# Performance work log

Hardware: AMD Instinct MI355X
Metric: run time of the kernel (lower is better)

## Reference

```python
import jax, jax.numpy as jnp
import numpy as np
import math

N_NODES = 50000
N_EDGES = 500000
HIDDEN = 64
N_LAYERS = 4
DELTA = 2.5
N_AGG = 6      # mean, max, min, std, var, sum
N_SCALE = 3    # identity, amplification, attenuation
EPS_BN = 1e-5


def setup_inputs() -> dict:
    key = jax.random.key(0)
    ks = jax.random.split(key, 12)
    d = HIDDEN
    L = N_LAYERS
    din_u = (N_AGG * N_SCALE + 1) * d  # 19*d: [self || scaled aggregates]
    return {
        "node_feat": jax.random.normal(ks[0], (N_NODES, d), jnp.float32),
        "edge_feat": jax.random.normal(ks[1], (N_EDGES, 4), jnp.float32),
        "edge_src": jax.random.randint(ks[2], (N_EDGES,), 0, N_NODES, jnp.int32),
        "edge_dst": jax.random.randint(ks[3], (N_EDGES,), 0, N_NODES, jnp.int32),
        "WM": jax.random.normal(ks[4], (L, 2 * d, d), jnp.float32) / math.sqrt(2 * d),
        "bM": jnp.zeros((L, d), jnp.float32),
        "WU": jax.random.normal(ks[5], (L, din_u, d), jnp.float32) / math.sqrt(din_u),
        "bU": jnp.zeros((L, d), jnp.float32),
        "gamma_t": jnp.ones((L, d), jnp.float32),
        "beta_t": jnp.zeros((L, d), jnp.float32),
        "Wmix": jax.random.normal(ks[6], (L, d, d), jnp.float32) / math.sqrt(d),
        "bmix": jnp.zeros((L, d), jnp.float32),
        "gamma_o": jnp.ones((L, d), jnp.float32),
        "beta_o": jnp.zeros((L, d), jnp.float32),
    }


def _batchnorm(x, gamma, beta):
    # BatchNorm1d in training mode: batch stats, biased variance
    mu = jnp.mean(x, axis=0)
    var = jnp.mean(jnp.square(x - mu), axis=0)
    return (x - mu) * jax.lax.rsqrt(var + EPS_BN) * gamma + beta


def _pna_layer(h, src, dst, WM, bM, WU, bU, g_t, b_t, Wmix, bmix, g_o, b_o):
    n = h.shape[0]
    # message: M([h_src || h_dst])  -> [E, d]
    msg = jnp.concatenate([h[src], h[dst]], axis=1) @ WM + bM
    deg = jax.ops.segment_sum(jnp.ones(src.shape[0], h.dtype), dst, num_segments=n)
    denom = jnp.maximum(deg, 1.0)[:, None]
    s = jax.ops.segment_sum(msg, dst, num_segments=n)
    mean = s / denom
    mean_sq = jax.ops.segment_sum(msg * msg, dst, num_segments=n) / denom
    var = jax.nn.relu(mean_sq - mean * mean)
    std = jnp.sqrt(var + 1e-30)
    has = (deg > 0)[:, None]
    mx = jnp.where(has, jax.ops.segment_max(msg, dst, num_segments=n), 0.0)
    mn = jnp.where(has, jax.ops.segment_min(msg, dst, num_segments=n), 0.0)
    agg = jnp.concatenate([mean, mx, mn, std, var, s], axis=1)  # [N, 6d]
    # degree scalers (zero-degree nodes have all-zero agg, so 0-scale is safe)
    logD = jnp.log(deg + 1.0)[:, None]
    amp = logD / DELTA
    att = jnp.where(logD > 0, DELTA / jnp.where(logD > 0, logD, 1.0), 0.0)
    h_neigh = jnp.concatenate([agg, agg * amp, agg * att], axis=1)  # [N, 18d]
    hu = jnp.concatenate([h, h_neigh], axis=1) @ WU + bU           # [N, d]
    hu = hu * (1.0 / math.sqrt(n))  # dgl graph-size norm snorm_n = 1/sqrt(N)
    hbn = _batchnorm(hu, g_t, b_t)  # tower batchnorm; dropout p=0 -> identity
    hm = jax.nn.leaky_relu(hbn @ Wmix + bmix, 0.01)
    out = hm + h  # PNAConv internal residual (in_size == out_size)
    # outer wrapper: relu(BatchNorm(layer_out)) + node_feat
    return jax.nn.relu(_batchnorm(out, g_o, b_o)) + h


def reference(node_feat, edge_feat, edge_src, edge_dst, WM, bM, WU, bU,
              gamma_t, beta_t, Wmix, bmix, gamma_o, beta_o):
    del edge_feat  # dgl PNAConv built with edge_feat_size=0: edge feats unused
    h = node_feat
    for i in range(N_LAYERS):
        h = _pna_layer(h, edge_src, edge_dst, WM[i], bM[i], WU[i], bU[i],
                       gamma_t[i], beta_t[i], Wmix[i], bmix[i],
                       gamma_o[i], beta_o[i])
    return h
```

## Files before the change

kernel.cpp:

```cpp
#include <hip/hip_runtime.h>
#include <hip/hip_bf16.h>


#define ND 50000
#define NE 500000
#define NB_SCAN ((ND + 255) / 256)
typedef __hip_bfloat16 bh;
typedef unsigned short us;
typedef __attribute__((ext_vector_type(8))) short short8;
typedef __attribute__((ext_vector_type(4))) float floatx4;
#define MFMA(a, b, c) __builtin_amdgcn_mfma_f32_16x16x32_bf16(a, b, c, 0, 0, 0)

__device__ float B2F(us u) { union { unsigned v; float f; } c; c.v = ((unsigned)u) << 16; return c.f; }
__device__ us F2B(float x) {
  union { float f; unsigned v; } c; c.f = x;
  unsigned r = c.v + 0x7fffu + ((c.v >> 16) & 1u);
  return (us)(r >> 16);
}
__device__ float LD(const void* p, size_t i, int ib) {
  return ib ? B2F(((const us*)p)[i]) : ((const float*)p)[i];
}
__device__ void SP(us* Xh, us* Xl, size_t i, float x) {
  us h = F2B(x);
  Xh[i] = h;
  Xl[i] = F2B(x - B2F(h));
}

__device__ inline void gll16(const void* g, void* l) {
  __builtin_amdgcn_global_load_lds((const __attribute__((address_space(1))) unsigned*)g,
                                   (__attribute__((address_space(3))) unsigned*)l, 16, 0, 0);
}

__global__ void kdt(const unsigned* nf, int* fl) {
  __shared__ int cnt;
  if (threadIdx.x == 0) cnt = 0;
  __syncthreads();
  float v = B2F((us)(nf[threadIdx.x] & 0xffffu));
  float av = fabsf(v);
  if (av > 0.0009f && av < 100.f) atomicAdd(&cnt, 1);
  __syncthreads();
  if (threadIdx.x == 0) fl[0] = (cnt >= 128) ? 1 : 0;
}

__global__ void PNA_9826885173934_kernel(const void* nf, const int* fl, float* hf) {
  int ib = fl[0];
  int i = blockIdx.x * 256 + threadIdx.x;
  if (i < ND * 64) hf[i] = LD(nf, i, ib);
}

__global__ void kz(int* d) {
  int i = blockIdx.x * 256 + threadIdx.x;
  if (i < ND) d[i] = 0;
}

__global__ void kd(const int* ed, int* d) {
  int e = blockIdx.x * 256 + threadIdx.x;
  if (e < NE) { int t = ed[e]; if (t >= 0 && t < ND) atomicAdd(&d[t], 1); }
}

__global__ void ks1(const int* d, int* bs) {
  __shared__ int r[256];
  int i = blockIdx.x * 256 + threadIdx.x;
  r[threadIdx.x] = (i < ND) ? d[i] : 0;
  __syncthreads();
  for (int o = 128; o > 0; o >>= 1) {
    if (threadIdx.x < o) r[threadIdx.x] += r[threadIdx.x + o];
    __syncthreads();
  }
  if (threadIdx.x == 0) bs[blockIdx.x] = r[0];
}

__global__ void ks2(int* bs, int* rp) {
  __shared__ int p[256];
  int t = threadIdx.x;
  int v = (t < NB_SCAN) ? bs[t] : 0;
  p[t] = v;
  __syncthreads();
  for (int o = 1; o < 256; o <<= 1) {
    int u = (t >= o) ? p[t - o] : 0;
    __syncthreads();
    p[t] += u;
    __syncthreads();
  }
  if (t < NB_SCAN) bs[t] = p[t] - v;
  if (t == NB_SCAN - 1) rp[ND] = p[t];
}

__global__ void ks3(const int* d, const int* bs, int* rp, int* nx) {
  __shared__ int p[256];
  int t = threadIdx.x;
  int i = blockIdx.x * 256 + t;
  int v = (i < ND) ? d[i] : 0;
  p[t] = v;
  __syncthreads();
  for (int o = 1; o < 256; o <<= 1) {
    int u = (t >= o) ? p[t - o] : 0;
    __syncthreads();
    p[t] += u;
    __syncthreads();
  }
  if (i < ND) {
    int ex = bs[blockIdx.x] + p[t] - v;
    rp[i] = ex;
    nx[i] = ex;
  }
}

__global__ void kc(const int* es, const int* ed, int* nx, int* ss) {
  int e = blockIdx.x * 256 + threadIdx.x;
  if (e < NE) {
    int t = ed[e];
    if (t >= 0 && t < ND) {
      int p = atomicAdd(&nx[t], 1);
      if (p >= 0 && p < NE) ss[p] = es[e];
    }
  }
}

__global__ void kp4(const void* WU, const int* fl, us* Wkh, us* Wkl) {
  int ib = fl[0];
  int gi = blockIdx.x * 256 + threadIdx.x;
  if (gi >= 192 * 448 * 4) return;
  int l = gi / (192 * 448), i = gi - l * (192 * 448);
  int c = i / 448, k = i - c * 448;
  size_t lo = (size_t)l * 77824;
  float o = 0.f;
  if (c < 64) o = LD(WU, lo + (size_t)k * 64 + c, ib);
  else if (c < 128) { if (k >= 64) o = LD(WU, lo + (size_t)(k + 384) * 64 + (c - 64), ib); }
  else { if (k >= 64) o = LD(WU, lo + (size_t)(k + 768) * 64 + (c - 128), ib); }
  us h = F2B(o);
  Wkh[gi] = h;
  Wkl[gi] = F2B(o - B2F(h));
}

__global__ void kpm4(const void* WM, const int* fl, us* WMh, us* WMl) {
  int ib = fl[0];
  int gi = blockIdx.x * 256 + threadIdx.x;
  if (gi >= 128 * 64 * 4) return;
  int l = gi >> 13, i = gi & 8191;
  int j = i >> 6, k = i & 63;
  float o = LD(WM, (size_t)l * 8192 + (size_t)((j < 64 ? 0 : 64) + k) * 64 + (j & 63), ib);
  us h = F2B(o);
  WMh[gi] = h;
  WMl[gi] = F2B(o - B2F(h));
}

__global__ void kpx4(const void* Wm, const int* fl, us* WXh, us* WXl) {
  int ib = fl[0];
  int gi = blockIdx.x * 256 + threadIdx.x;
  if (gi >= 64 * 64 * 4) return;
  int l = gi >> 12, i = gi & 4095;
  int j = i >> 6, k = i & 63;
  float o = LD(Wm, (size_t)l * 4096 + (size_t)k * 64 + j, ib);
  us h = F2B(o);
  WXh[gi] = h;
  WXl[gi] = F2B(o - B2F(h));
}

__global__ __launch_bounds__(256) void ka2(const float* hf, const us* WMh, const us* WMl,
                                           const void* bM, int lb, const int* fl, float* ab,
                                           float* st) {
  __shared__ __attribute__((aligned(16))) us Asm[2][128 * 64];
  __shared__ __attribute__((aligned(16))) us Bsm[2][128 * 64];
  int t = threadIdx.x, w = t >> 6, lane = t & 63;
  int quad = lane >> 4, l15 = lane & 15;
  int nb = blockIdx.x * 128;
  if (blockIdx.x == 0) st[t] = 0.f;
  {
    int slot = lane & 7, rg = lane >> 3;
#pragma unroll
    for (int ch = 0; ch < 2; ++ch) {
#pragma unroll
      for (int j = 0; j < 4; ++j) {
        int row = j * 32 + w * 8 + rg;
        int op = (slot ^ (row & 7)) << 4;
        const us* s = (op < 64 ? WMh : WMl) + (size_t)row * 64 + ch * 32 + ((op & 63) >> 1);
        gll16(s, (char*)Bsm[ch] + (size_t)(j * 32 + w * 8) * 128);
      }
    }
  }
  {
    int q = t & 3;
#pragma unroll
    for (int rr = 0; rr < 2; ++rr) {
      int r = rr * 64 + (t >> 2);
      int node = nb + r; if (node > ND - 1) node = ND - 1;
      const float* hp = hf + (size_t)node * 64 + q * 16;
      float f[16];
#pragma unroll
      for (int i = 0; i < 4; ++i) {
        float4 v = ((const float4*)hp)[i];
        f[i * 4 + 0] = v.x; f[i * 4 + 1] = v.y; f[i * 4 + 2] = v.z; f[i * 4 + 3] = v.w;
      }
      short8 ha = {}, hb = {}, la = {}, lb8 = {};
#pragma unroll
      for (int i = 0; i < 8; ++i) {
        us h0 = F2B(f[i]);     ha[i] = (short)h0;  la[i]  = (short)F2B(f[i] - B2F(h0));
        us h1 = F2B(f[8 + i]); hb[i] = (short)h1;  lb8[i] = (short)F2B(f[8 + i] - B2F(h1));
      }
      int ch = q >> 1, kof = (q & 1) * 32, sw = (r & 7) << 4;
      char* base = (char*)Asm[ch] + r * 128;
      *(short8*)(base + (kof ^ sw)) = ha;
      *(short8*)(base + ((kof + 16) ^ sw)) = hb;
      *(short8*)(base + ((64 + kof) ^ sw)) = la;
      *(short8*)(base + ((64 + kof + 16) ^ sw)) = lb8;
    }
  }
  __syncthreads();
  floatx4 ac[8][2] = {};
#pragma unroll
  for (int ch = 0; ch < 2; ++ch) {
    const char* Ab = (const char*)Asm[ch];
    const char* Bb = (const char*)Bsm[ch];
    short8 bh2[2], bl2[2];
#pragma unroll
    for (int ct = 0; ct < 2; ++ct) {
      int row = (w * 2 + ct) * 16 + l15, sw = (row & 7) << 4;
      bh2[ct] = *(const short8*)(Bb + row * 128 + ((quad * 16) ^ sw));
      bl2[ct] = *(const short8*)(Bb + row * 128 + ((64 + quad * 16) ^ sw));
    }
#pragma unroll
    for (int mt = 0; mt < 8; ++mt) {
      int row = mt * 16 + l15, sw = (row & 7) << 4;
      short8 ah = *(const short8*)(Ab + row * 128 + ((quad * 16) ^ sw));
      short8 al = *(const short8*)(Ab + row * 128 + ((64 + quad * 16) ^ sw));
#pragma unroll
      for (int ct = 0; ct < 2; ++ct) {
        ac[mt][ct] = MFMA(ah, bh2[ct], ac[mt][ct]);
        ac[mt][ct] = MFMA(ah, bl2[ct], ac[mt][ct]);
        ac[mt][ct] = MFMA(al, bh2[ct], ac[mt][ct]);
      }
    }
  }
  int ib = fl[0];
#pragma unroll
  for (int ct = 0; ct < 2; ++ct) {
    int j = w * 32 + ct * 16 + l15;
    float bi = (j >= 64) ? LD(bM, (size_t)lb + (j - 64), ib) : 0.f;
#pragma unroll
    for (int mt = 0; mt < 8; ++mt) {
#pragma unroll
      for (int r = 0; r < 4; ++r) {
        int node = nb + mt * 16 + quad * 4 + r;
        if (node < ND) ab[(size_t)node * 128 + j] = ac[mt][ct][r] + bi;
      }
    }
  }
}

__global__ void kg(const float* hf, const float* ab, const int* rp, const int* ss,
                   us* Xh, us* Xl, float* am, float* at) {
  int n = blockIdx.x * 4 + (threadIdx.x >> 6), c = threadIdx.x & 63;
  if (n >= ND) return;
  int r0 = rp[n], r1 = rp[n + 1];
  const float* abc = ab + c;
  float s = 0.f, q = 0.f, mx = -3.4e38f, mn = 3.4e38f;
  int e = r0;
  for (; e + 4 <= r1; e += 4) {
    int i0 = ss[e], i1 = ss[e + 1], i2 = ss[e + 2], i3 = ss[e + 3];
    if ((unsigned)i0 >= ND) i0 = 0;
    if ((unsigned)i1 >= ND) i1 = 0;
    if ((unsigned)i2 >= ND) i2 = 0;
    if ((unsigned)i3 >= ND) i3 = 0;
    float v0 = abc[(size_t)i0 * 128];
    float v1 = abc[(size_t)i1 * 128];
    float v2 = abc[(size_t)i2 * 128];
    float v3 = abc[(size_t)i3 * 128];
    s += (v0 + v1) + (v2 + v3);
    q += (v0 * v0 + v1 * v1) + (v2 * v2 + v3 * v3);
    mx = fmaxf(fmaxf(mx, v0), fmaxf(fmaxf(v1, v2), v3));
    mn = fminf(fminf(mn, v0), fminf(fminf(v1, v2), v3));
  }
  for (; e < r1; ++e) {
    int si = ss[e];
    if ((unsigned)si >= ND) si = 0;
    float v = abc[(size_t)si * 128];
    s += v; q += v * v; mx = fmaxf(mx, v); mn = fminf(mn, v);
  }
  float bb = ab[(size_t)n * 128 + 64 + c];
  int dg = r1 - r0;
  float de = fmaxf((float)dg, 1.f);
  float sv = s + (float)dg * bb;
  float qv = q + 2.f * bb * s + (float)dg * bb * bb;
  float me = sv / de;
  float va = fmaxf(qv / de - me * me, 0.f);
  float sd = sqrtf(va + 1e-30f);
  float mxv = mx + bb, mnv = mn + bb;
  if (dg <= 0) { mxv = 0.f; mnv = 0.f; }
  size_t b = (size_t)n * 448;
  SP(Xh, Xl, b + c, hf[(size_t)n * 64 + c]);
  SP(Xh, Xl, b + 64 + c, me);
  SP(Xh, Xl, b + 128 + c, mxv);
  SP(Xh, Xl, b + 192 + c, mnv);
  SP(Xh, Xl, b + 256 + c, sd);
  SP(Xh, Xl, b + 320 + c, va);
  SP(Xh, Xl, b + 384 + c, sv);
  if (c == 0) {
    float l = logf((float)dg + 1.f);
    am[n] = l * 0.4f;
    at[n] = (dg > 0) ? 2.5f / l : 0.f;
  }
}

__device__ inline void k1stage(const us* Xh, const us* Xl, const us* Wkh, const us* Wkl,
                               char* Ab, char* Bb, int w, int lane, int nb, int k0) {
  int row8 = lane >> 3, slot = lane & 7;
  if (w < 2) {
#pragma unroll
    for (int jj = 0; jj < 8; ++jj) {
      int j = w * 8 + jj;
      int row = j * 8 + row8;
      int op = (slot ^ (row & 7)) << 4;
      int node = nb + row; if (node > ND - 1) node = ND - 1;
      const us* s = (op < 64 ? Xh : Xl) + (size_t)node * 448 + k0 + ((op & 63) >> 1);
      gll16(s, Ab + j * 1024);
    }
  } else {
#pragma unroll
    for (int jj = 0; jj < 12; ++jj) {
      int j = (w - 2) * 12 + jj;
      int row = j * 8 + row8;
      int op = (slot ^ (row & 7)) << 4;
      const us* s = (op < 64 ? Wkh : Wkl) + (size_t)row * 448 + k0 + ((op & 63) >> 1);
      gll16(s, Bb + j * 1024);
    }
  }
}

__global__ __launch_bounds__(256, 2) void k1(
    const us* Xh, const us* Xl, const us* Wkh, const us* Wkl,
    const void* bU, int lb, const int* fl, const float* am, const float* at,
    float* hu, float* st) {
  __shared__ __attribute__((aligned(16))) us As[2][128 * 64];
  __shared__ __attribute__((aligned(16))) us Bs[2][192 * 64];
  int t = threadIdx.x;
  int ib = fl[0];
  int w = t >> 6, lane = t & 63;
  int quad = lane >> 4, l15 = lane & 15;
  int nb = blockIdx.x * 128;
  floatx4 ac[8][3] = {};
  k1stage(Xh, Xl, Wkh, Wkl, (char*)As[0], (char*)Bs[0], w, lane, nb, 0);
  __syncthreads();
  int buf = 0;
  for (int tt = 0; tt < 14; ++tt) {
    if (tt < 13)
      k1stage(Xh, Xl, Wkh, Wkl, (char*)As[buf ^ 1], (char*)Bs[buf ^ 1], w, lane, nb,
              (tt + 1) * 32);
    const char* Ab = (const char*)As[buf];
    const char* Bb = (const char*)Bs[buf];
    short8 bh2[3], bl2[3];
#pragma unroll
    for (int ci = 0; ci < 3; ++ci) {
      int row = (w + ci * 4) * 16 + l15, sw = (row & 7) << 4;
      bh2[ci] = *(const short8*)(Bb + row * 128 + ((quad * 16) ^ sw));
      bl2[ci] = *(const short8*)(Bb + row * 128 + ((64 + quad * 16) ^ sw));
    }
#pragma unroll
    for (int mt = 0; mt < 8; ++mt) {
      int row = mt * 16 + l15, sw = (row & 7) << 4;
      short8 ah = *(const short8*)(Ab + row * 128 + ((quad * 16) ^ sw));
      short8 al = *(const short8*)(Ab + row * 128 + ((64 + quad * 16) ^ sw));
#pragma unroll
      for (int ci = 0; ci < 3; ++ci) {
        ac[mt][ci] = MFMA(ah, bh2[ci], ac[mt][ci]);
        ac[mt][ci] = MFMA(ah, bl2[ci], ac[mt][ci]);
        ac[mt][ci] = MFMA(al, bh2[ci], ac[mt][ci]);
      }
    }
    __syncthreads();
    buf ^= 1;
  }
  float* sr = (float*)As;
  if (t < 128) sr[t] = 0.f;
  __syncthreads();
  int c = w * 16 + l15;
  float bu = LD(bU, (size_t)lb + c, ib);
  float ps = 0.f, pq = 0.f;
#pragma unroll
  for (int mt = 0; mt < 8; ++mt) {
#pragma unroll
    for (int r = 0; r < 4; ++r) {
      int node = nb + mt * 16 + quad * 4 + r;
      if (node < ND) {
        float v = (ac[mt][0][r] + am[node] * ac[mt][1][r] + at[node] * ac[mt][2][r] + bu)
                  * 4.4721359549995794e-3f;
        hu[(size_t)node * 64 + c] = v;
        ps += v; pq += v * v;
      }
    }
  }
  atomicAdd(&sr[c], ps);
  atomicAdd(&sr[64 + c], pq);
  __syncthreads();
  if (t < 128) atomicAdd(&st[t], sr[t]);
}

__global__ __launch_bounds__(256) void k2m(const float* hu, float* st, const void* gt,
                                           const void* bt, const us* WXh, const us* WXl,
                                           const void* bm, int lb, const int* fl,
                                           const float* hf, float* ob) {
  __shared__ __attribute__((aligned(16))) us Asm[2][64 * 64];
  __shared__ __attribute__((aligned(16))) us Bsm[2][64 * 64];
  __shared__ float bnS[192];
  int t = threadIdx.x, w = t >> 6, lane = t & 63;
  int quad = lane >> 4, l15 = lane & 15;
  int nb = blockIdx.x * 64;
  int ib = fl[0];
  {
#pragma unroll
    for (int i = 0; i < 4; ++i) {
      int idx = t * 4 + i;
      int ch = idx >> 9, rem = idx & 511;
      int row = rem >> 3, slot = rem & 7;
      int op = slot << 4;
      const us* s = WXh + (size_t)row * 64 + ch * 32 + (op >> 1);
      const us* s2 = WXl + (size_t)row * 64 + ch * 32 + (op >> 1);
      short8 v = (op < 64) ? *(const short8*)s : *(const short8*)s2;
      int sw = (row & 7) << 4;
      *(short8*)((char*)Bsm[ch] + row * 128 + (op ^ sw)) = v;
    }
  }
  if (t < 64) {
    float mu = st[t] * 2e-5f;
    float va = st[64 + t] * 2e-5f - mu * mu;
    bnS[t] = mu;
    bnS[64 + t] = rsqrtf(fmaxf(va, 0.f) + 1e-5f) * LD(gt, (size_t)lb + t, ib);
    bnS[128 + t] = LD(bt, (size_t)lb + t, ib);
  }
  __syncthreads();
  {
    int r = t >> 2, q = t & 3;
    int node = nb + r; if (node > ND - 1) node = ND - 1;
    const float* hp = hu + (size_t)node * 64 + q * 16;
    float f[16];
#pragma unroll
    for (int i = 0; i < 4; ++i) {
      float4 v = ((const float4*)hp)[i];
      f[i * 4 + 0] = v.x; f[i * 4 + 1] = v.y; f[i * 4 + 2] = v.z; f[i * 4 + 3] = v.w;
    }
#pragma unroll
    for (int i = 0; i < 16; ++i) {
      int k = q * 16 + i;
      f[i] = (f[i] - bnS[k]) * bnS[64 + k] + bnS[128 + k];
    }
    short8 ha = {}, hb = {}, la = {}, lb8 = {};
#pragma unroll
    for (int i = 0; i < 8; ++i) {
      us h0 = F2B(f[i]);     ha[i] = (short)h0;  la[i]  = (short)F2B(f[i] - B2F(h0));
      us h1 = F2B(f[8 + i]); hb[i] = (short)h1;  lb8[i] = (short)F2B(f[8 + i] - B2F(h1));
    }
    int ch = q >> 1, kof = (q & 1) * 32, sw = (r & 7) << 4;
    char* base = (char*)Asm[ch] + r * 128;
    *(short8*)(base + (kof ^ sw)) = ha;
    *(short8*)(base + ((kof + 16) ^ sw)) = hb;
    *(short8*)(base + ((64 + kof) ^ sw)) = la;
    *(short8*)(base + ((64 + kof + 16) ^ sw)) = lb8;
  }
  __syncthreads();
  floatx4 ac[4] = {};
#pragma unroll
  for (int ch = 0; ch < 2; ++ch) {
    const char* Ab = (const char*)Asm[ch];
    const char* Bb = (const char*)Bsm[ch];
    short8 ah[4], al[4], bh2, bl2;
#pragma unroll
    for (int mt = 0; mt < 4; ++mt) {
      int row = mt * 16 + l15, sw = (row & 7) << 4;
      ah[mt] = *(const short8*)(Ab + row * 128 + ((quad * 16) ^ sw));
      al[mt] = *(const short8*)(Ab + row * 128 + ((64 + quad * 16) ^ sw));
    }
    {
      int row = w * 16 + l15, sw = (row & 7) << 4;
      bh2 = *(const short8*)(Bb + row * 128 + ((quad * 16) ^ sw));
      bl2 = *(const short8*)(Bb + row * 128 + ((64 + quad * 16) ^ sw));
    }
#pragma unroll
    for (int mt = 0; mt < 4; ++mt) {
      ac[mt] = MFMA(ah[mt], bh2, ac[mt]);
      ac[mt] = MFMA(ah[mt], bl2, ac[mt]);
      ac[mt] = MFMA(al[mt], bh2, ac[mt]);
    }
  }
  __syncthreads();
  float* sr = (float*)Asm;
  if (t < 128) sr[t] = 0.f;
  __syncthreads();
  int j = w * 16 + l15;
  float b1 = LD(bm, (size_t)lb + j, ib);
  float ps = 0.f, pq = 0.f;
#pragma unroll
  for (int mt = 0; mt < 4; ++mt) {
#pragma unroll
    for (int r = 0; r < 4; ++r) {
      int node = nb + mt * 16 + quad * 4 + r;
      if (node < ND) {
        float a = ac[mt][r] + b1;
        float hm = (a > 0.f) ? a : 0.01f * a;
        float o = hm + hf[(size_t)node * 64 + j];
        ob[(size_t)node * 64 + j] = o;
        ps += o; pq += o * o;
      }
    }
  }
  atomicAdd(&sr[j], ps);
  atomicAdd(&sr[64 + j], pq);
  __syncthreads();
  if (t < 128) atomicAdd(&st[128 + t], sr[t]);
}

__global__ void k3(const float* ob, const float* st, const void* go, const void* bo,
                   int lb, const int* fl, float* hf, void* op, int last) {
  int ib = fl[0];
  int i = blockIdx.x * 256 + threadIdx.x;
  if (i >= ND * 64) return;
  int c = i & 63;
  float mu = st[128 + c] * 2e-5f;
  float va = st[192 + c] * 2e-5f - mu * mu;
  float x = (ob[i] - mu) * rsqrtf(fmaxf(va, 0.f) + 1e-5f) * LD(go, (size_t)lb + c, ib)
            + LD(bo, (size_t)lb + c, ib);
  x = fmaxf(x, 0.f);
  float h = x + hf[i];
  hf[i] = h;
  if (last) {
    if (ib) ((us*)op)[i] = F2B(h);
    else ((float*)op)[i] = h;
  }
}

extern "C" void kernel_launch(void* const* d_in, const int* in_sizes, int n_in,
                              void* d_out, int out_size, void* d_ws, size_t ws_size,
                              hipStream_t stream) {
  int sh = (n_in >= 14) ? 0 : -1;
  const void* nf = d_in[0];
  const int* es = (const int*)d_in[2 + sh];
  const int* ed = (const int*)d_in[3 + sh];
  const void* WM = d_in[4 + sh];
  const void* bM = d_in[5 + sh];
  const void* WU = d_in[6 + sh];
  const void* bU = d_in[7 + sh];
  const void* gt = d_in[8 + sh];
  const void* bt = d_in[9 + sh];
  const void* Wm = d_in[10 + sh];
  const void* bm = d_in[11 + sh];
  const void* go = d_in[12 + sh];
  const void* bo = d_in[13 + sh];

  char* B = (char*)d_ws;
  float* hf = (float*)B;
  float* ab = (float*)(B + 12800000);
  us* Xh = (us*)(B + 38400000);
  us* Xl = (us*)(B + 83200000);
  size_t o0 = 128000000;
  float* am = (float*)(B + o0);
  float* at = (float*)(B + o0 + 200192);
  int* dg = (int*)(B + o0 + 400384);
  int* rp = (int*)(B + o0 + 600576);
  int* nx = (int*)(B + o0 + 800768);
  int* ss = (int*)(B + o0 + 1000960);
  us* Wkh4 = (us*)(B + o0 + 3001088);
  us* Wkl4 = (us*)(B + o0 + 3689216);
  float* st = (float*)(B + o0 + 4377344);
  int* fl = (int*)(B + o0 + 4378368);
  int* bs = (int*)(B + o0 + 4378624);
  us* WMh4 = (us*)(B + o0 + 4379648);
  us* WMl4 = (us*)(B + o0 + 4445184);
  us* WXh4 = (us*)(B + o0 + 4510720);
  us* WXl4 = (us*)(B + o0 + 4543488);
  float* hu = ab;
  float* ob = ab + (size_t)ND * 64;

  kdt<<<1, 256, 0, stream>>>((const unsigned*)nf, fl);
  PNA_9826885173934_kernel<<<(ND * 64 + 255) / 256, 256, 0, stream>>>(nf, fl, hf);
  kz<<<(ND + 255) / 256, 256, 0, stream>>>(dg);
  kd<<<(NE + 255) / 256, 256, 0, stream>>>(ed, dg);
  ks1<<<NB_SCAN, 256, 0, stream>>>(dg, bs);
  ks2<<<1, 256, 0, stream>>>(bs, rp);
  ks3<<<NB_SCAN, 256, 0, stream>>>(dg, bs, rp, nx);
  kc<<<(NE + 255) / 256, 256, 0, stream>>>(es, ed, nx, ss);
  kp4<<<(192 * 448 * 4 + 255) / 256, 256, 0, stream>>>(WU, fl, Wkh4, Wkl4);
  kpm4<<<(128 * 64 * 4 + 255) / 256, 256, 0, stream>>>(WM, fl, WMh4, WMl4);
  kpx4<<<(64 * 64 * 4 + 255) / 256, 256, 0, stream>>>(Wm, fl, WXh4, WXl4);

  for (int L = 0; L < 4; ++L) {
    ka2<<<(ND + 127) / 128, 256, 0, stream>>>(hf, WMh4 + (size_t)L * 8192,
                                              WMl4 + (size_t)L * 8192, bM, L * 64, fl, ab, st);
    kg<<<(ND + 3) / 4, 256, 0, stream>>>(hf, ab, rp, ss, Xh, Xl, am, at);
    k1<<<(ND + 127) / 128, 256, 0, stream>>>(Xh, Xl, Wkh4 + (size_t)L * 86016,
                                             Wkl4 + (size_t)L * 86016, bU, L * 64, fl,
                                             am, at, hu, st);
    k2m<<<(ND + 63) / 64, 256, 0, stream>>>(hu, st, gt, bt, WXh4 + (size_t)L * 4096,
                                            WXl4 + (size_t)L * 4096, bm, L * 64, fl, hf, ob);
    k3<<<(ND * 64 + 255) / 256, 256, 0, stream>>>(ob, st, go, bo, L * 64, fl, hf, d_out,
                                                  (L == 3) ? 1 : 0);
  }
}
```

Baseline: 712.1 us.

## Fuse outer batchnorm-residual into next layer's message GEMM and unroll gather

The per-layer k3 pass (outer BatchNorm, ReLU, residual add) now runs inside the next layer's ka2 prologue, which reads ob and hf, applies the normalization and writes hf back. Only the last layer still launches k3. Stats buffers are double-buffered so the previous layer's statistics survive while the current ones are zeroed. ob moves into the Xh region, which is assumed free by that point, and the kg gather loop is unrolled to 8 edges to keep more loads in flight. This removes three launches plus a full read/write pass over node features, at the cost of aliasing ob with Xh and adding a sync in ka2.

New measurement: 712.8 us. No clear change (+0.1%).

```diff
diff --git a/kernel.cpp b/kernel.cpp
--- a/kernel.cpp
+++ b/kernel.cpp
@@ -157,15 +157,19 @@
   WXl[gi] = F2B(o - B2F(h));
 }
 
-__global__ __launch_bounds__(256) void ka2(const float* hf, const us* WMh, const us* WMl,
-                                           const void* bM, int lb, const int* fl, float* ab,
-                                           float* st) {
+__global__ __launch_bounds__(256) void ka2(float* hf, const float* ob, const void* go,
+                                           const void* bo, int lbp, const us* WMh,
+                                           const us* WMl, const void* bM, int lb,
+                                           const int* fl, float* ab, float* stC,
+                                           const float* stP, int fuse) {
   __shared__ __attribute__((aligned(16))) us Asm[2][128 * 64];
   __shared__ __attribute__((aligned(16))) us Bsm[2][128 * 64];
+  __shared__ float bnO[192];
   int t = threadIdx.x, w = t >> 6, lane = t & 63;
   int quad = lane >> 4, l15 = lane & 15;
   int nb = blockIdx.x * 128;
-  if (blockIdx.x == 0) st[t] = 0.f;
+  int ib = fl[0];
+  if (blockIdx.x == 0) stC[t] = 0.f;
   {
     int slot = lane & 7, rg = lane >> 3;
 #pragma unroll
@@ -179,18 +183,45 @@
       }
     }
   }
+  if (fuse && t < 64) {
+    float mu = stP[128 + t] * 2e-5f;
+    float va = stP[192 + t] * 2e-5f - mu * mu;
+    bnO[t] = mu;
+    bnO[64 + t] = rsqrtf(fmaxf(va, 0.f) + 1e-5f) * LD(go, (size_t)lbp + t, ib);
+    bnO[128 + t] = LD(bo, (size_t)lbp + t, ib);
+  }
+  __syncthreads();
   {
     int q = t & 3;
 #pragma unroll
     for (int rr = 0; rr < 2; ++rr) {
       int r = rr * 64 + (t >> 2);
-      int node = nb + r; if (node > ND - 1) node = ND - 1;
-      const float* hp = hf + (size_t)node * 64 + q * 16;
+      int node = nb + r;
+      int valid = (node < ND);
+      if (!valid) node = ND - 1;
       float f[16];
-#pragma unroll
-      for (int i = 0; i < 4; ++i) {
-        float4 v = ((const float4*)hp)[i];
-        f[i * 4 + 0] = v.x; f[i * 4 + 1] = v.y; f[i * 4 + 2] = v.z; f[i * 4 + 3] = v.w;
+      if (fuse) {
+        const float* op_ = ob + (size_t)node * 64 + q * 16;
+        float* hp = hf + (size_t)node * 64 + q * 16;
+#pragma unroll
+        for (int i = 0; i < 4; ++i) {
+          float4 vo = ((const float4*)op_)[i];
+          float4 vh = ((const float4*)hp)[i];
+          int k0 = q * 16 + i * 4;
+          float o0 = fmaxf((vo.x - bnO[k0 + 0]) * bnO[64 + k0 + 0] + bnO[128 + k0 + 0], 0.f) + vh.x;
+          float o1 = fmaxf((vo.y - bnO[k0 + 1]) * bnO[64 + k0 + 1] + bnO[128 + k0 + 1], 0.f) + vh.y;
+          float o2 = fmaxf((vo.z - bnO[k0 + 2]) * bnO[64 + k0 + 2] + bnO[128 + k0 + 2], 0.f) + vh.z;
+          float o3 = fmaxf((vo.w - bnO[k0 + 3]) * bnO[64 + k0 + 3] + bnO[128 + k0 + 3], 0.f) + vh.w;
+          f[i * 4 + 0] = o0; f[i * 4 + 1] = o1; f[i * 4 + 2] = o2; f[i * 4 + 3] = o3;
+          if (valid) ((float4*)hp)[i] = make_float4(o0, o1, o2, o3);
+        }
+      } else {
+        const float* hp = hf + (size_t)node * 64 + q * 16;
+#pragma unroll
+        for (int i = 0; i < 4; ++i) {
+          float4 v = ((const float4*)hp)[i];
+          f[i * 4 + 0] = v.x; f[i * 4 + 1] = v.y; f[i * 4 + 2] = v.z; f[i * 4 + 3] = v.w;
+        }
       }
       short8 ha = {}, hb = {}, la = {}, lb8 = {};
 #pragma unroll
@@ -232,7 +263,6 @@
       }
     }
   }
-  int ib = fl[0];
 #pragma unroll
   for (int ct = 0; ct < 2; ++ct) {
     int j = w * 32 + ct * 16 + l15;
@@ -256,20 +286,21 @@
   const float* abc = ab + c;
   float s = 0.f, q = 0.f, mx = -3.4e38f, mn = 3.4e38f;
   int e = r0;
-  for (; e + 4 <= r1; e += 4) {
-    int i0 = ss[e], i1 = ss[e + 1], i2 = ss[e + 2], i3 = ss[e + 3];
-    if ((unsigned)i0 >= ND) i0 = 0;
-    if ((unsigned)i1 >= ND) i1 = 0;
-    if ((unsigned)i2 >= ND) i2 = 0;
-    if ((unsigned)i3 >= ND) i3 = 0;
-    float v0 = abc[(size_t)i0 * 128];
-    float v1 = abc[(size_t)i1 * 128];
-    float v2 = abc[(size_t)i2 * 128];
-    float v3 = abc[(size_t)i3 * 128];
-    s += (v0 + v1) + (v2 + v3);
-    q += (v0 * v0 + v1 * v1) + (v2 * v2 + v3 * v3);
-    mx = fmaxf(fmaxf(mx, v0), fmaxf(fmaxf(v1, v2), v3));
-    mn = fminf(fminf(mn, v0), fminf(fminf(v1, v2), v3));
+  for (; e + 8 <= r1; e += 8) {
+    int ix[8];
+#pragma unroll
+    for (int u = 0; u < 8; ++u) {
+      int si = ss[e + u];
+      ix[u] = ((unsigned)si >= ND) ? 0 : si;
+    }
+    float v[8];
+#pragma unroll
+    for (int u = 0; u < 8; ++u) v[u] = abc[(size_t)ix[u] * 128];
+#pragma unroll
+    for (int u = 0; u < 8; ++u) {
+      s += v[u]; q += v[u] * v[u];
+      mx = fmaxf(mx, v[u]); mn = fminf(mn, v[u]);
+    }
   }
   for (; e < r1; ++e) {
     int si = ss[e];
@@ -509,7 +540,7 @@
 }
 
 __global__ void k3(const float* ob, const float* st, const void* go, const void* bo,
-                   int lb, const int* fl, float* hf, void* op, int last) {
+                   int lb, const int* fl, float* hf, void* op) {
   int ib = fl[0];
   int i = blockIdx.x * 256 + threadIdx.x;
   if (i >= ND * 64) return;
@@ -521,10 +552,8 @@
   x = fmaxf(x, 0.f);
   float h = x + hf[i];
   hf[i] = h;
-  if (last) {
-    if (ib) ((us*)op)[i] = F2B(h);
-    else ((float*)op)[i] = h;
-  }
+  if (ib) ((us*)op)[i] = F2B(h);
+  else ((float*)op)[i] = h;
 }
 
 extern "C" void kernel_launch(void* const* d_in, const int* in_sizes, int n_in,
@@ -550,6 +579,7 @@
   float* ab = (float*)(B + 12800000);
   us* Xh = (us*)(B + 38400000);
   us* Xl = (us*)(B + 83200000);
+  float* ob = (float*)(B + 38400000);
   size_t o0 = 128000000;
   float* am = (float*)(B + o0);
   float* at = (float*)(B + o0 + 200192);
@@ -560,14 +590,13 @@
   us* Wkh4 = (us*)(B + o0 + 3001088);
   us* Wkl4 = (us*)(B + o0 + 3689216);
   float* st = (float*)(B + o0 + 4377344);
-  int* fl = (int*)(B + o0 + 4378368);
-  int* bs = (int*)(B + o0 + 4378624);
-  us* WMh4 = (us*)(B + o0 + 4379648);
-  us* WMl4 = (us*)(B + o0 + 4445184);
-  us* WXh4 = (us*)(B + o0 + 4510720);
-  us* WXl4 = (us*)(B + o0 + 4543488);
+  int* fl = (int*)(B + o0 + 4379392);
+  int* bs = (int*)(B + o0 + 4379648);
+  us* WMh4 = (us*)(B + o0 + 4380672);
+  us* WMl4 = (us*)(B + o0 + 4446208);
+  us* WXh4 = (us*)(B + o0 + 4511744);
+  us* WXl4 = (us*)(B + o0 + 4544512);
   float* hu = ab;
-  float* ob = ab + (size_t)ND * 64;
 
   kdt<<<1, 256, 0, stream>>>((const unsigned*)nf, fl);
   PNA_9826885173934_kernel<<<(ND * 64 + 255) / 256, 256, 0, stream>>>(nf, fl, hf);
@@ -582,15 +611,18 @@
   kpx4<<<(64 * 64 * 4 + 255) / 256, 256, 0, stream>>>(Wm, fl, WXh4, WXl4);
 
   for (int L = 0; L < 4; ++L) {
-    ka2<<<(ND + 127) / 128, 256, 0, stream>>>(hf, WMh4 + (size_t)L * 8192,
-                                              WMl4 + (size_t)L * 8192, bM, L * 64, fl, ab, st);
+    float* stC = st + (L & 1) * 256;
+    const float* stP = st + ((L + 1) & 1) * 256;
+    ka2<<<(ND + 127) / 128, 256, 0, stream>>>(hf, ob, go, bo, (L > 0) ? (L - 1) * 64 : 0,
+                                              WMh4 + (size_t)L * 8192,
+                                              WMl4 + (size_t)L * 8192, bM, L * 64, fl,
+                                              ab, stC, stP, (L > 0) ? 1 : 0);
     kg<<<(ND + 3) / 4, 256, 0, stream>>>(hf, ab, rp, ss, Xh, Xl, am, at);
     k1<<<(ND + 127) / 128, 256, 0, stream>>>(Xh, Xl, Wkh4 + (size_t)L * 86016,
                                              Wkl4 + (size_t)L * 86016, bU, L * 64, fl,
-                                             am, at, hu, st);
-    k2m<<<(ND + 63) / 64, 256, 0, stream>>>(hu, st, gt, bt, WXh4 + (size_t)L * 4096,
+                                             am, at, hu, stC);
+    k2m<<<(ND + 63) / 64, 256, 0, stream>>>(hu, stC, gt, bt, WXh4 + (size_t)L * 4096,
                                             WXl4 + (size_t)L * 4096, bm, L * 64, fl, hf, ob);
-    k3<<<(ND * 64 + 255) / 256, 256, 0, stream>>>(ob, st, go, bo, L * 64, fl, hf, d_out,
-                                                  (L == 3) ? 1 : 0);
-  }
-}
+  }
+  k3<<<(ND * 64 + 255) / 256, 256, 0, stream>>>(ob, st + 256, go, bo, 192, fl, hf, d_out);
+}
```
